# Kernel optimization log

Measured on AMD Instinct MI355X. Metric: run time of the kernel, lower is better.

Reference implementation:

```python
import jax, jax.numpy as jnp
import numpy as np

N_WIRES = 14
N_LAYERS = 2
BATCH = 128


def _ry(t):
    # t: scalar or (B,) real angle -> (...,2,2) complex64 RY matrix
    c = jnp.cos(t / 2)
    s = jnp.sin(t / 2)
    m = jnp.stack([jnp.stack([c, -s], -1), jnp.stack([s, c], -1)], -2)
    return m.astype(jnp.complex64)


def _rz(t):
    tc = t.astype(jnp.complex64) if hasattr(t, 'astype') else jnp.asarray(t, jnp.complex64)
    em = jnp.exp(-0.5j * tc)
    ep = jnp.exp(0.5j * tc)
    z = jnp.zeros_like(em)
    return jnp.stack([jnp.stack([em, z], -1), jnp.stack([z, ep], -1)], -2)


def _rx(t):
    c = jnp.cos(t / 2).astype(jnp.complex64)
    s = (-1j) * jnp.sin(t / 2).astype(jnp.complex64)
    return jnp.stack([jnp.stack([c, s], -1), jnp.stack([s, c], -1)], -2)


def _apply_1q(state, mat, w, n):
    # state: (B, 2**n), wire 0 = most significant axis (Pennylane convention)
    B = state.shape[0]
    s = state.reshape(B, 2 ** w, 2, -1)
    if mat.ndim == 2:
        s = jnp.einsum('ij,bajc->baic', mat, s)
    else:  # per-batch matrices (data encoding)
        s = jnp.einsum('bij,bajc->baic', mat, s)
    return s.reshape(B, -1)


def _apply_cnot(state, c, t, n):
    B = state.shape[0]
    p, q = (c, t) if c < t else (t, c)
    s = state.reshape(B, 2 ** p, 2, 2 ** (q - p - 1), 2, 2 ** (n - q - 1))
    if c < t:
        # control at axis 2, target at axis 4; flip target where control==1
        s = jnp.stack([s[:, :, 0], jnp.flip(s[:, :, 1], axis=3)], axis=2)
    else:
        # control at axis 4, target at axis 2
        s = jnp.stack([s[:, :, :, :, 0], jnp.flip(s[:, :, :, :, 1], axis=2)], axis=4)
    return s.reshape(B, -1)


def _circuit(x, params):
    B, n = x.shape
    n_layers = params.shape[0]
    state = jnp.zeros((B, 2 ** n), dtype=jnp.complex64).at[:, 0].set(1.0)
    # data encoding: RY(x[:, w]) on each wire (batched gate matrices)
    for w in range(n):
        state = _apply_1q(state, _ry(x[:, w]), w, n)
    for l in range(n_layers):
        for w in range(n):
            state = _apply_1q(state, _ry(params[l, w, 0]), w, n)
            state = _apply_1q(state, _rz(params[l, w, 1]), w, n)
            state = _apply_1q(state, _rx(params[l, w, 2]), w, n)
        for w in range(n - 1):
            state = _apply_cnot(state, w, w + 1, n)
        state = _apply_cnot(state, n - 1, 0, n)
    probs = state.real ** 2 + state.imag ** 2  # (B, 2**n)
    zs = []
    for w in range(n):
        p = probs.reshape(B, 2 ** w, 2, -1)
        zs.append(p[:, :, 0].sum(axis=(1, 2)) - p[:, :, 1].sum(axis=(1, 2)))
    return jnp.stack(zs, axis=1).astype(jnp.float32)  # (B, n) <Z_w>


def setup_inputs() -> dict:
    key = jax.random.key(0)
    kx, kp = jax.random.split(key)
    x = jax.random.normal(kx, (BATCH, N_WIRES), dtype=jnp.float32)
    params = jax.random.normal(kp, (N_LAYERS, N_WIRES, 3), dtype=jnp.float32)
    return {"x": x, "params": params}


def reference(x, params):
    return _circuit(x, params)
```

## Files before the change

### kernel.cpp

```cpp
#include <hip/hip_runtime.h>

#define NW 14
#define NT 1024
#define BATCH 128

typedef float v2f __attribute__((ext_vector_type(2)));

constexpr unsigned cnot_pc(unsigned j, int c, int t) {
  int pc = 13 - c, pt = 13 - t;
  return j ^ (((j >> pc) & 1u) << pt);
}
constexpr unsigned gperm(unsigned j) {
  j = cnot_pc(j, 13, 0);
  for (int w = 12; w >= 0; --w) j = cnot_pc(j, w, w + 1);
  return j;
}
constexpr int pcnt(unsigned x) {
  int c = 0;
  while (x) { c += (int)(x & 1u); x >>= 1; }
  return c;
}

struct CT {
  unsigned M[NW], S[NW], R[NW];
  static constexpr void inv(const unsigned col[NW], unsigned out[NW]) {
    unsigned rm[NW] = {}, ri[NW] = {};
    for (int r = 0; r < NW; ++r) { rm[r] = 0; ri[r] = 1u << r; }
    for (int b = 0; b < NW; ++b)
      for (int r = 0; r < NW; ++r) rm[r] |= ((col[b] >> r) & 1u) << b;
    for (int c = 0; c < NW; ++c) {
      int piv = c;
      while (!((rm[piv] >> c) & 1u)) ++piv;
      unsigned tm = rm[c]; rm[c] = rm[piv]; rm[piv] = tm;
      unsigned ti = ri[c]; ri[c] = ri[piv]; ri[piv] = ti;
      for (int r = 0; r < NW; ++r)
        if (r != c && ((rm[r] >> c) & 1u)) { rm[r] ^= rm[c]; ri[r] ^= ri[c]; }
    }
    for (int r = 0; r < NW; ++r) out[r] = ri[r];
  }
  constexpr CT() : M{}, S{}, R{} {
    unsigned c1[NW] = {}, c2[NW] = {};
    for (int b = 0; b < NW; ++b) { c1[b] = gperm(1u << b); c2[b] = gperm(c1[b]); }
    unsigned i1[NW] = {}, i2[NW] = {};
    inv(c1, i1); inv(c2, i2);
    for (int w = 0; w < NW; ++w) { M[w] = c1[13 - w]; S[w] = i1[13 - w]; R[w] = i2[13 - w]; }
  }
};
static constexpr CT qct{};
static_assert(qct.M[0] == 0x3000u && qct.M[12] == 0x3u && qct.M[13] == 0x3001u, "mask check");

constexpr unsigned p1f(unsigned b) {
  return ((b ^ (b >> 1)) ^ ((b & 1u) * 0x3000u)) & 0x3FFFu;
}
constexpr bool chk_p1_formula() {
  for (unsigned b = 0; b < 16384u; ++b)
    if (p1f(b) != gperm(b)) return false;
  return true;
}
static_assert(chk_p1_formula(), "P1 closed form == gperm");
constexpr bool chk_role() {
  for (int w = 0; w < NW; ++w) {
    for (unsigned b = 0; b < 16384u; b += 37u)
      if ((unsigned)(pcnt(p1f(b) & qct.S[w]) & 1) != ((b >> (13 - w)) & 1u)) return false;
    for (int j = 0; j < 14; ++j)
      if ((unsigned)(pcnt(p1f(1u << j) & qct.S[w]) & 1) != (((1u << j) >> (13 - w)) & 1u))
        return false;
  }
  return true;
}
static_assert(chk_role(), "b-space role = storage bit");
struct RBt {
  unsigned v[NW];
  constexpr RBt() : v{} {
    for (int w = 0; w < NW; ++w) {
      unsigned m = 0;
      for (int j = 0; j < 14; ++j)
        if (pcnt(gperm(1u << j) & qct.R[w]) & 1) m |= 1u << j;
      v[w] = m;
    }
  }
};
static constexpr RBt rbt{};
constexpr bool chk_meas() {
  for (int w = 0; w < NW; ++w)
    for (unsigned b = 0; b < 16384u; b += 41u)
      if ((pcnt(p1f(b) & qct.R[w]) & 1) != (pcnt(b & rbt.v[w]) & 1)) return false;
  return true;
}
static_assert(chk_meas(), "b-space measurement masks");
constexpr bool chk_cr() {
  for (unsigned r = 0; r < 16u; ++r)
    if (p1f(r << 1) != ((r << 1) ^ r) || p1f(r << 1) >= 128u) return false;
  return true;
}
static_assert(chk_cr(), "P1(r<<1) == (r<<1)^r and < 128");

__device__ __forceinline__ v2f vswap(v2f m) {
  v2f r;
  r.x = -m.y;
  r.y = m.x;
  return r;
}
__device__ __forceinline__ v2f cmulv(v2f a, v2f b) {
  v2f r;
  r.x = fmaf(a.x, b.x, -a.y * b.y);
  r.y = fmaf(a.x, b.y, a.y * b.x);
  return r;
}

__device__ __forceinline__ void make_mat(float ay, float az, float ax_, v2f m[4]) {
  float c, s, ct, st, cr, sr;
  __sincosf(0.5f * ay, &s, &c);
  __sincosf(0.5f * az, &st, &ct);
  __sincosf(0.5f * ax_, &sr, &cr);
  v2f em, ep;
  em.x = ct; em.y = -st;
  ep.x = ct; ep.y = st;
  v2f r00 = c * em, r01 = -s * em, r10 = s * ep, r11 = c * ep;
  v2f isr;
  isr.x = 0.f; isr.y = -sr;
  m[0] = cmulv(isr, r10) + cr * r00;
  m[1] = cmulv(isr, r11) + cr * r01;
  m[2] = cmulv(isr, r00) + cr * r10;
  m[3] = cmulv(isr, r01) + cr * r11;
}

template <int CTRL> __device__ __forceinline__ int dppi(int x) {
  return __builtin_amdgcn_update_dpp(0, x, CTRL, 0xF, 0xF, true);
}
template <unsigned LM> __device__ __forceinline__ float lane_xor1(float x) {
  if constexpr (LM == 0u) return x;
  else if constexpr (LM >= 16u) {
    return __shfl_xor(x, (int)LM, 64);
  } else {
    int v = __float_as_int(x);
    if constexpr ((LM & 0xCu) == 0xCu) v = dppi<0x140>(v);
    else if constexpr ((LM & 0xCu) == 0x4u) v = dppi<0x141>(v);
    else if constexpr ((LM & 0xCu) == 0x8u) v = dppi<0x128>(v);
    constexpr unsigned REM = ((LM & 0xCu) == 0xCu)   ? (LM ^ 0xFu)
                             : ((LM & 0xCu) == 0x4u) ? (LM ^ 0x7u)
                             : ((LM & 0xCu) == 0x8u) ? (LM ^ 0x8u)
                                                     : LM;
    if constexpr (REM != 0u) {
      constexpr int QC = (int)((0u ^ REM) | ((1u ^ REM) << 2) | ((2u ^ REM) << 4) |
                               ((3u ^ REM) << 6));
      v = dppi<QC>(v);
    }
    return __int_as_float(v);
  }
}
template <unsigned LM> __device__ __forceinline__ v2f lane_xor2(v2f v) {
  if constexpr (LM == 0u) return v;
  v2f r;
  r.x = lane_xor1<LM>(v.x);
  r.y = lane_xor1<LM>(v.y);
  return r;
}


template <unsigned RM>
__device__ __forceinline__ void gate_reg(v2f (&a)[16], const float4* G) {
  const float4 A0 = G[0], A1 = G[1], A2 = G[2], A3 = G[3];
  v2f m00, m01, m10, m11, s00, s01, s10, s11;
  m00.x = A0.x; m00.y = A0.y; m01.x = A0.z; m01.y = A0.w;
  m10.x = A1.x; m10.y = A1.y; m11.x = A1.z; m11.y = A1.w;
  s00.x = A2.x; s00.y = A2.y; s01.x = A2.z; s01.y = A2.w;
  s10.x = A3.x; s10.y = A3.y; s11.x = A3.z; s11.y = A3.w;
#pragma unroll
  for (int r = 0; r < 16; ++r) {
    if (r & (int)RM) continue;
    const int r1 = r | (int)RM;
    const v2f A = a[r], B = a[r1];
    a[r] = A.x * m00 + A.y * s00 + B.x * m01 + B.y * s01;
    a[r1] = A.x * m10 + A.y * s10 + B.x * m11 + B.y * s11;
  }
}

template <unsigned LM>
__device__ __forceinline__ void gate_dpp(v2f (&a)[16], const float4* G, bool role) {
  const float4 A0 = G[0], A1 = G[1], A2 = G[2], A3 = G[3];
  v2f m00, m01, m10, m11, s00, s01, s10, s11;
  m00.x = A0.x; m00.y = A0.y; m01.x = A0.z; m01.y = A0.w;
  m10.x = A1.x; m10.y = A1.y; m11.x = A1.z; m11.y = A1.w;
  s00.x = A2.x; s00.y = A2.y; s01.x = A2.z; s01.y = A2.w;
  s10.x = A3.x; s10.y = A3.y; s11.x = A3.z; s11.y = A3.w;
  const v2f f0 = role ? m11 : m00, f0s = role ? s11 : s00;
  const v2f f1 = role ? m10 : m01, f1s = role ? s10 : s01;
#pragma unroll
  for (int r = 0; r < 16; ++r) {
    const v2f P = lane_xor2<LM>(a[r]);
    const v2f A = a[r];
    a[r] = A.x * f0 + A.y * f0s + P.x * f1 + P.y * f1s;
  }
}

__global__ __launch_bounds__(NT, 4) void qsim(const float* __restrict__ x,
                                              const float* __restrict__ params,
                                              float* __restrict__ out) {
  __shared__ v2f stx[16384];
  __shared__ v2f v0[NW][2];
  __shared__ float4 gq[NW][4];
  __shared__ v2f Ahi[128];
  __shared__ v2f BloP[8][17];
  __shared__ float red[16][NW];

  const int bat = blockIdx.x;
  const int t = threadIdx.x;
  const unsigned ln = (unsigned)t & 63u, wv = (unsigned)t >> 6;

  if (t < 2 * NW) {
    const int layer = (t >= NW);
    const int w = t - layer * NW;
    v2f m[4];
    if (!layer) {
      make_mat(params[w * 3 + 0] + x[bat * NW + w], params[w * 3 + 1], params[w * 3 + 2], m);
      v0[w][0] = m[0];
      v0[w][1] = m[2];
    } else {
      make_mat(params[NW * 3 + w * 3 + 0], params[NW * 3 + w * 3 + 1],
               params[NW * 3 + w * 3 + 2], m);
      const v2f s0 = vswap(m[0]), s1 = vswap(m[1]), s2 = vswap(m[2]), s3 = vswap(m[3]);
      gq[w][0] = make_float4(m[0].x, m[0].y, m[1].x, m[1].y);
      gq[w][1] = make_float4(m[2].x, m[2].y, m[3].x, m[3].y);
      gq[w][2] = make_float4(s0.x, s0.y, s1.x, s1.y);
      gq[w][3] = make_float4(s2.x, s2.y, s3.x, s3.y);
    }
  }
  __syncthreads();
  if (t < 128) {
    v2f pa; pa.x = 1.f; pa.y = 0.f;
#pragma unroll
    for (int w = 0; w < 7; ++w) pa = cmulv(pa, v0[w][(t >> (6 - w)) & 1]);
    Ahi[t] = pa;
    v2f pb; pb.x = 1.f; pb.y = 0.f;
#pragma unroll
    for (int w = 7; w < 14; ++w) pb = cmulv(pb, v0[w][(t >> (13 - w)) & 1]);
    BloP[t >> 4][t & 15] = pb;
  }
  __syncthreads();

  const unsigned bb = (ln << 5) | ((wv & 7u) << 11) | (wv >> 3);
  const unsigned qb = ((bb ^ (bb >> 1)) ^ ((bb & 1u) * 0x3000u)) & 0x3FFFu;

  v2f a[16];
  {
    const v2f ahi = Ahi[qb >> 7];
    const v2f ahis = vswap(ahi);
    const unsigned q7 = qb & 127u;
#pragma unroll
    for (int r = 0; r < 16; ++r) {
      const unsigned j = q7 ^ (((unsigned)r << 1) ^ (unsigned)r);
      const v2f b = BloP[j >> 4][j & 15u];
      a[r] = b.x * ahi + b.y * ahis;
    }
  }

  gate_reg<1>(a, gq[12]);
  gate_reg<2>(a, gq[11]);
  gate_reg<4>(a, gq[10]);
  gate_reg<8>(a, gq[9]);
  gate_dpp<1>(a, gq[8], (ln & 1u) != 0);
  gate_dpp<2>(a, gq[7], (ln & 2u) != 0);
  gate_dpp<4>(a, gq[6], (ln & 4u) != 0);
  gate_dpp<8>(a, gq[5], (ln & 8u) != 0);

  {
    const unsigned bw = bb ^ ((ln & 0xFu) << 1);
#pragma unroll
    for (int r = 0; r < 16; ++r) stx[bw ^ ((unsigned)r << 1)] = a[r];
  }
  __syncthreads();
  const unsigned brb = (wv << 1) | (((ln >> 2) & 0xFu) << 5) | ((ln & 1u) << 9) |
                       (((ln >> 1) & 1u) << 10);
  {
    const unsigned br = brb ^ (((brb >> 5) & 0xFu) << 1);
#pragma unroll
    for (int r = 0; r < 16; ++r)
      a[r] = stx[br | (((unsigned)r & 7u) << 11) | ((unsigned)r >> 3)];
  }

  gate_dpp<1>(a, gq[4], (ln & 1u) != 0);
  gate_dpp<2>(a, gq[3], (ln & 2u) != 0);
  gate_reg<1>(a, gq[2]);
  gate_reg<2>(a, gq[1]);
  gate_reg<4>(a, gq[0]);
  gate_reg<8>(a, gq[13]);

  float T[16];
#pragma unroll
  for (int r = 0; r < 16; ++r) T[r] = fmaf(a[r].x, a[r].x, a[r].y * a[r].y);
#pragma unroll
  for (int s = 1; s < 16; s <<= 1) {
#pragma unroll
    for (int r = 0; r < 16; ++r) {
      if (!(r & s)) {
        float u = T[r], v = T[r ^ s];
        T[r] = u + v;
        T[r ^ s] = u - v;
      }
    }
  }

#pragma unroll
  for (int w = 0; w < NW; ++w) {
    constexpr unsigned Rr[NW] = {rbt.v[0], rbt.v[1], rbt.v[2], rbt.v[3], rbt.v[4],
                                 rbt.v[5], rbt.v[6], rbt.v[7], rbt.v[8], rbt.v[9],
                                 rbt.v[10], rbt.v[11], rbt.v[12], rbt.v[13]};
    const unsigned R = Rr[w];
    const unsigned m = ((R >> 11) & 1u) | (((R >> 12) & 1u) << 1) | (((R >> 13) & 1u) << 2) |
                       ((R & 1u) << 3);
    float val = T[m];
    val = (__popc(brb & R) & 1) ? -val : val;
    val += lane_xor1<1>(val);
    val += lane_xor1<2>(val);
    { float u = lane_xor1<4>(val); val += u; }
    val += lane_xor1<8>(val);
    val += __shfl_xor(val, 16, 64);
    val += __shfl_xor(val, 32, 64);
    if ((t & 63) == 0) red[wv][w] = val;
  }
  __syncthreads();
  if (t < NW) {
    float s = 0.f;
#pragma unroll
    for (int i = 0; i < 16; ++i) s += red[i][t];
    out[bat * NW + t] = s;
  }
}

extern "C" void kernel_launch(void* const* d_in, const int* in_sizes, int n_in,
                              void* d_out, int out_size, void* d_ws, size_t ws_size,
                              hipStream_t stream) {
  (void)in_sizes; (void)n_in; (void)d_ws; (void)ws_size; (void)out_size;
  const float* x = (const float*)d_in[0];
  const float* params = (const float*)d_in[1];
  float* out = (float*)d_out;
  qsim<<<dim3(BATCH), dim3(NT), 0, stream>>>(x, params, out);
}
```

Before: 68.29 us.

## Replace full statevector simulation with analytic product-state chain contraction

Adds a qchain kernel that uses the fact that the first layer yields a product state and the CNOT ring is a permutation. Each <Z_w> is computed as a small 2x2 transfer-matrix contraction along the 14 wires, so the 16K-amplitude state is never stored per batch. One 64-thread block per batch element replaces 1024-thread blocks doing full state updates. The derivation is checked at compile time on random small cases, and the launcher falls back to qsim if that check fails. It relies on the structure of this circuit (2 layers, product-state encoding), which is fixed by the task.

```diff
diff --git a/kernel.cpp b/kernel.cpp
--- a/kernel.cpp
+++ b/kernel.cpp
@@ -95,6 +95,101 @@
 }
 static_assert(chk_cr(), "P1(r<<1) == (r<<1)^r and < 128");
 
+template <class T> struct cx { T re, im; };
+template <class T> __host__ __device__ constexpr cx<T> operator+(cx<T> a, cx<T> b) {
+  return {a.re + b.re, a.im + b.im};
+}
+template <class T> __host__ __device__ constexpr cx<T> operator-(cx<T> a, cx<T> b) {
+  return {a.re - b.re, a.im - b.im};
+}
+template <class T> __host__ __device__ constexpr cx<T> operator*(cx<T> a, cx<T> b) {
+  return {a.re * b.re - a.im * b.im, a.re * b.im + a.im * b.re};
+}
+template <class T> __host__ __device__ constexpr cx<T> cj(cx<T> a) { return {a.re, -a.im}; }
+
+template <int N, class T, class FS, class FM>
+__host__ __device__ constexpr cx<T> contract_case(const FS& s, const FM& M, int cb, int cp) {
+  cx<T> v[2][2] = {};
+  for (int q = 0; q < 2; ++q)
+    for (int qp = 0; qp < 2; ++qp)
+      v[q][qp] = s(0, q) * cj(s(0, qp)) * M(0, qp ^ cp, q ^ cb);
+#pragma unroll
+  for (int j = 1; j <= N - 2; ++j) {
+    cx<T> A[2][2] = {}, B[2][2] = {};
+    for (int p = 0; p < 2; ++p) {
+      A[p][0] = cj(s(j, 0)) * v[p][0] + cj(s(j, 1)) * v[p][1];
+      A[p][1] = cj(s(j, 1)) * v[p][0] + cj(s(j, 0)) * v[p][1];
+    }
+    for (int qp = 0; qp < 2; ++qp) {
+      B[0][qp] = s(j, 0) * A[0][qp] + s(j, 1) * A[1][qp];
+      B[1][qp] = s(j, 1) * A[0][qp] + s(j, 0) * A[1][qp];
+    }
+    for (int q = 0; q < 2; ++q)
+      for (int qp = 0; qp < 2; ++qp)
+        v[q][qp] = M(j, qp, q) * B[q][qp];
+  }
+  cx<T> e{0, 0};
+  for (int p = 0; p < 2; ++p)
+    for (int pp = 0; pp < 2; ++pp)
+      e = e + s(N - 1, cb ^ p) * cj(s(N - 1, cp ^ pp)) * v[p][pp];
+  return M(N - 1, cp, cb) * e;
+}
+
+template <int N> constexpr bool chain_check() {
+  cx<double> S[N][2] = {};
+  cx<double> MM[N][2][2] = {};
+  unsigned st8 = 12345u + (unsigned)N * 977u;
+  auto nxt = [&st8]() {
+    st8 = st8 * 1664525u + 1013904223u;
+    return ((double)(st8 >> 8) / 8388608.0) - 1.0;
+  };
+  for (int j = 0; j < N; ++j) {
+    S[j][0] = {nxt(), nxt()};
+    S[j][1] = {nxt(), nxt()};
+    for (int r = 0; r < 2; ++r)
+      for (int c = 0; c < 2; ++c) MM[j][r][c] = {nxt(), nxt()};
+  }
+  const int SZ = 1 << N;
+  cx<double> phi[1 << N] = {}, tmp[1 << N] = {};
+  for (int q = 0; q < SZ; ++q) {
+    cx<double> a{1, 0};
+    for (int j = 0; j < N; ++j) a = a * S[j][(q >> (N - 1 - j)) & 1];
+    phi[q] = a;
+  }
+  for (int g = 0; g < N; ++g) {
+    const int c = (g < N - 1) ? g : (N - 1);
+    const int t = (g < N - 1) ? (g + 1) : 0;
+    for (int q = 0; q < SZ; ++q)
+      tmp[q] = phi[q ^ ((((q >> (N - 1 - c)) & 1)) << (N - 1 - t))];
+    for (int q = 0; q < SZ; ++q) phi[q] = tmp[q];
+  }
+  cx<double> mp[1 << N] = {};
+  for (int q = 0; q < SZ; ++q) mp[q] = phi[q];
+  for (int j = 0; j < N; ++j) {
+    const int bit = 1 << (N - 1 - j);
+    for (int q = 0; q < SZ; ++q) {
+      if (q & bit) continue;
+      cx<double> a0 = mp[q], a1 = mp[q | bit];
+      mp[q] = MM[j][0][0] * a0 + MM[j][0][1] * a1;
+      mp[q | bit] = MM[j][1][0] * a0 + MM[j][1][1] * a1;
+    }
+  }
+  cx<double> E{0, 0};
+  for (int q = 0; q < SZ; ++q) E = E + cj(phi[q]) * mp[q];
+  auto sg = [&S](int j, int b) { return S[j][b]; };
+  auto mg = [&MM](int j, int r, int c) { return MM[j][r][c]; };
+  cx<double> Tt{0, 0};
+  for (int cb = 0; cb < 2; ++cb)
+    for (int cp = 0; cp < 2; ++cp)
+      Tt = Tt + contract_case<N, double>(sg, mg, cb, cp);
+  double dr = Tt.re - E.re, di = Tt.im - E.im;
+  if (dr < 0) dr = -dr;
+  if (di < 0) di = -di;
+  double mag = (E.re < 0 ? -E.re : E.re) + (E.im < 0 ? -E.im : E.im) + 1.0;
+  return (dr + di) < 1e-9 * mag;
+}
+constexpr bool CHAIN_OK = chain_check<4>() && chain_check<5>() && chain_check<6>();
+
 __device__ __forceinline__ v2f vswap(v2f m) {
   v2f r;
   r.x = -m.y;
@@ -107,7 +202,6 @@
   r.y = fmaf(a.x, b.y, a.y * b.x);
   return r;
 }
-
 __device__ __forceinline__ void make_mat(float ay, float az, float ax_, v2f m[4]) {
   float c, s, ct, st, cr, sr;
   __sincosf(0.5f * ay, &s, &c);
@@ -124,7 +218,6 @@
   m[2] = cmulv(isr, r00) + cr * r10;
   m[3] = cmulv(isr, r01) + cr * r11;
 }
-
 template <int CTRL> __device__ __forceinline__ int dppi(int x) {
   return __builtin_amdgcn_update_dpp(0, x, CTRL, 0xF, 0xF, true);
 }
@@ -157,6 +250,52 @@
   return r;
 }
 
+using cxf = cx<float>;
+__global__ __launch_bounds__(64) void qchain(const float* __restrict__ x,
+                                             const float* __restrict__ params,
+                                             float* __restrict__ out) {
+  __shared__ cxf Ssh[NW][2];
+  __shared__ cxf Msh[NW][2][2];
+
+  const int bat = blockIdx.x;
+  const int t = threadIdx.x;
+
+  if (t < NW) {
+    v2f m[4];
+    make_mat(params[t * 3 + 0] + x[bat * NW + t], params[t * 3 + 1], params[t * 3 + 2], m);
+    Ssh[t][0] = {m[0].x, m[0].y};
+    Ssh[t][1] = {m[2].x, m[2].y};
+  } else if (t < 2 * NW) {
+    const int j = t - NW;
+    v2f m[4];
+    make_mat(params[NW * 3 + j * 3 + 0], params[NW * 3 + j * 3 + 1],
+             params[NW * 3 + j * 3 + 2], m);
+    const cxf g00{m[0].x, m[0].y}, g01{m[1].x, m[1].y};
+    const cxf g10{m[2].x, m[2].y}, g11{m[3].x, m[3].y};
+    Msh[j][0][0] = cj(g00) * g00 - cj(g10) * g10;
+    Msh[j][0][1] = cj(g00) * g01 - cj(g10) * g11;
+    Msh[j][1][0] = cj(g01) * g00 - cj(g11) * g10;
+    Msh[j][1][1] = cj(g01) * g01 - cj(g11) * g11;
+  }
+  __syncthreads();
+
+  const int w = t >> 2, c = t & 3;
+  if (w < NW) {
+    const unsigned Sm = qct.S[w];
+    auto sg = [&](int j, int b) { return Ssh[j][b]; };
+    auto mg = [&](int j, int r, int cc) {
+      const bool inS = (Sm >> (13 - j)) & 1u;
+      const cxf I = (r == cc) ? cxf{1.f, 0.f} : cxf{0.f, 0.f};
+      const cxf F = Msh[j][r][cc];
+      return inS ? F : I;
+    };
+    const cxf E = contract_case<NW, float>(sg, mg, c & 1, c >> 1);
+    float r = E.re;
+    r += lane_xor1<1>(r);
+    r += lane_xor1<2>(r);
+    if (c == 0) out[bat * NW + w] = r;
+  }
+}
 
 template <unsigned RM>
 __device__ __forceinline__ void gate_reg(v2f (&a)[16], const float4* G) {
@@ -175,7 +314,6 @@
     a[r1] = A.x * m10 + A.y * s10 + B.x * m11 + B.y * s11;
   }
 }
-
 template <unsigned LM>
 __device__ __forceinline__ void gate_dpp(v2f (&a)[16], const float4* G, bool role) {
   const float4 A0 = G[0], A1 = G[1], A2 = G[2], A3 = G[3];
@@ -335,5 +473,9 @@
   const float* x = (const float*)d_in[0];
   const float* params = (const float*)d_in[1];
   float* out = (float*)d_out;
-  qsim<<<dim3(BATCH), dim3(NT), 0, stream>>>(x, params, out);
-}
+  if constexpr (CHAIN_OK) {
+    qchain<<<dim3(BATCH), dim3(64), 0, stream>>>(x, params, out);
+  } else {
+    qsim<<<dim3(BATCH), dim3(NT), 0, stream>>>(x, params, out);
+  }
+}
```

Result: faster. 57.86 us (-15.3%).
